# Kernel tuning notes

Measured on AMD Instinct MI355X. Metric: run time of the kernel, lower is better.

## Reference

```python
import jax, jax.numpy as jnp
import numpy as np

B, S, C, H, W = 8, 64, 3, 224, 224   # batch, n_segments, channels, height, width
E, P = 128, 16                        # embed_dim, patch size of feature extractor


def _conv(x, w, b, stride, padding):
    y = jax.lax.conv_general_dilated(
        x, w, (stride, stride), padding,
        dimension_numbers=('NCHW', 'OIHW', 'NCHW'))
    return y + b[None, :, None, None]


def setup_inputs() -> dict:
    key = jax.random.key(0)
    k1, k2, k3 = jax.random.split(key, 3)
    img = jax.random.normal(k1, (B, C, H, W), jnp.float32)
    # SpixelNet stand-in: 3x3 conv -> n_segments logit channels
    w_spixel = jax.random.normal(k2, (S, C, 3, 3), jnp.float32) * 0.1
    b_spixel = jnp.zeros((S,), jnp.float32)
    # feature extractor stand-in: 16x16/16 patch conv -> embed_dim, then GAP
    w_patch = jax.random.normal(k3, (E, C, P, P), jnp.float32) * 0.02
    b_patch = jnp.zeros((E,), jnp.float32)
    return dict(img=img, w_spixel=w_spixel, b_spixel=b_spixel,
                w_patch=w_patch, b_patch=b_patch)


def reference(img, w_spixel, b_spixel, w_patch, b_patch):
    # superpixel tokenizer -> segment logits, argmax -> hard labels
    logits = _conv(img, w_spixel, b_spixel, 1, 'SAME')          # [B,S,H,W]
    labels = jnp.argmax(logits, axis=1)                          # [B,H,W] int

    # replicate per-batch torch.unique (sorted unique labels, zero-padded)
    flat = labels.reshape(B, -1)
    present = jnp.zeros((B, S), bool).at[jnp.arange(B)[:, None], flat].set(True)
    vals = jnp.where(present, jnp.arange(S)[None, :], S)
    uniq = jnp.sort(vals, axis=1)                                # uniques first
    uniq = jnp.where(uniq < S, uniq, 0)                          # pad with 0 like torch.zeros

    # broadcast-compare mask build + masked extract (the memory-bound op)
    mask = (labels[:, None, :, :] == uniq[:, :, None, None]).astype(img.dtype)  # [B,S,H,W]
    seg = (img[:, None, :, :, :] * mask[:, :, None, :, :]).reshape(B * S, C, H, W)

    # feature extractor: patch conv + global average pool
    feat = _conv(seg, w_patch, b_patch, P, 'VALID')              # [B*S,E,H/P,W/P]
    feat = feat.mean(axis=(2, 3))                                # [B*S,E]
    return feat.reshape(B, S, E)
```

## Files before the change

### kernel.cpp

```cpp
#include <hip/hip_runtime.h>

#define BD 8
#define SD 64
#define CD 3
#define HD 224
#define WD 224
#define ED 128
#define PD 16
#define HWD (HD*WD)
#define KD (CD*PD*PD)
#define PRT 8
#define CHK (HWD/PRT)

__device__ float              g_part[BD * CD * PRT * SD * 256];
__device__ int                g_labels[BD * HWD];
__device__ unsigned long long g_ppres[BD * PRT];

__global__ __launch_bounds__(256) void k_labels(
    const float* __restrict__ img,
    const float* __restrict__ wsp,
    const float* __restrict__ bsp)
{
    const int p = blockIdx.x * 256 + threadIdx.x;
    const int b = blockIdx.y;
    const int h = p / WD;
    const int w = p - h * WD;

    const float* ib = img + (size_t)b * CD * HWD;
    float pix[27];
    #pragma unroll
    for (int c = 0; c < 3; ++c)
        #pragma unroll
        for (int dh = 0; dh < 3; ++dh)
            #pragma unroll
            for (int dw = 0; dw < 3; ++dw) {
                int hh = h + dh - 1, ww = w + dw - 1;
                bool ok = (hh >= 0) & (hh < HD) & (ww >= 0) & (ww < WD);
                pix[(c * 3 + dh) * 3 + dw] = ok ? ib[c * HWD + hh * WD + ww] : 0.f;
            }

    float best = -INFINITY;
    int bi = 0;
    for (int s = 0; s < SD; ++s) {
        const float* wr = wsp + s * 27;
        float acc = bsp[s];
        #pragma unroll
        for (int j = 0; j < 27; ++j) acc = fmaf(pix[j], wr[j], acc);
        if (acc > best) { best = acc; bi = s; }
    }
    g_labels[b * HWD + p] = bi;
}

__global__ __launch_bounds__(256) void k_hist(const float* __restrict__ img)
{
    const int part = blockIdx.x, c = blockIdx.y, b = blockIdx.z;
    const int tid = threadIdx.x;

    __shared__ float acc[SD * 256];
    __shared__ unsigned long long pm;
    #pragma unroll
    for (int k = 0; k < 16; ++k)
        ((float4*)acc)[k * 256 + tid] = make_float4(0.f, 0.f, 0.f, 0.f);
    if (tid == 0) pm = 0ull;
    __syncthreads();

    const int start = part * CHK;
    const int*   lb = g_labels + (size_t)b * HWD;
    const float* ic = img + ((size_t)b * CD + c) * HWD;

    unsigned long long m = 0ull;
    for (int p = start + tid; p < start + CHK; p += 256) {
        const int lab = lb[p];
        const int h = p / WD, w = p - h * WD;
        const int cell = ((h & 15) << 4) | (w & 15);
        atomicAdd(&acc[lab * 256 + cell], ic[p]);
        m |= 1ull << lab;
    }
    #pragma unroll
    for (int d = 1; d < 64; d <<= 1) m |= __shfl_xor(m, d, 64);
    if ((tid & 63) == 0) atomicOr(&pm, m);
    __syncthreads();

    float4* dst = (float4*)(g_part + (((size_t)(b * CD + c)) * PRT + part) * (SD * 256));
    #pragma unroll
    for (int k = 0; k < 16; ++k)
        dst[k * 256 + tid] = ((float4*)acc)[k * 256 + tid];
    if (c == 0 && tid == 0) g_ppres[b * PRT + part] = pm;
}

__global__ __launch_bounds__(256) void k_out(
    const float* __restrict__ wp,
    const float* __restrict__ bp,
    float* __restrict__ out)
{
    __shared__ float4 gs4[KD / 4];
    const int i = blockIdx.x;
    const int b = blockIdx.y;
    const int tid = threadIdx.x;
    const int lane = tid & 63;
    const int wv = tid >> 6;

    unsigned long long m = 0ull;
    #pragma unroll
    for (int p2 = 0; p2 < PRT; ++p2) m |= g_ppres[b * PRT + p2];

    int l = 0;
    if (i < __popcll(m)) {
        unsigned long long mm = m;
        for (int t = 0; t < i; ++t) mm &= mm - 1;
        l = __builtin_ctzll(mm);
    }

    if (tid < KD / 4) {
        const int c = tid >> 6, cell4 = tid & 63;
        const float4* src = (const float4*)g_part
            + ((size_t)(b * CD + c) * PRT) * 4096 + l * 64 + cell4;
        float4 s = src[0];
        #pragma unroll
        for (int p2 = 1; p2 < PRT; ++p2) {
            float4 v = src[(size_t)p2 * 4096];
            s.x += v.x; s.y += v.y; s.z += v.z; s.w += v.w;
        }
        gs4[tid] = s;
    }
    __syncthreads();

    const float4 g0 = gs4[lane], g1 = gs4[lane + 64], g2 = gs4[lane + 128];

    #pragma unroll 4
    for (int j = 0; j < 32; ++j) {
        const int e = wv * 32 + j;
        const float4* wr = (const float4*)(wp + (size_t)e * KD);
        float4 a0 = wr[lane], a1 = wr[lane + 64], a2 = wr[lane + 128];
        float acc = g0.x * a0.x;
        acc = fmaf(g0.y, a0.y, acc); acc = fmaf(g0.z, a0.z, acc); acc = fmaf(g0.w, a0.w, acc);
        acc = fmaf(g1.x, a1.x, acc); acc = fmaf(g1.y, a1.y, acc);
        acc = fmaf(g1.z, a1.z, acc); acc = fmaf(g1.w, a1.w, acc);
        acc = fmaf(g2.x, a2.x, acc); acc = fmaf(g2.y, a2.y, acc);
        acc = fmaf(g2.z, a2.z, acc); acc = fmaf(g2.w, a2.w, acc);
        #pragma unroll
        for (int off = 32; off; off >>= 1) acc += __shfl_xor(acc, off, 64);
        if (lane == 0)
            out[(size_t)(b * SD + i) * ED + e] = bp[e] + acc * (1.f / 196.f);
    }
}

extern "C" void kernel_launch(void* const* d_in, const int* in_sizes, int n_in,
                              void* d_out, int out_size, void* d_ws, size_t ws_size,
                              hipStream_t stream) {
    const float *img = nullptr, *wsp = nullptr, *bsp = nullptr, *wp = nullptr, *bp = nullptr;
    for (int i = 0; i < n_in; ++i) {
        switch (in_sizes[i]) {
            case BD * CD * HWD:      img = (const float*)d_in[i]; break;
            case SD * CD * 9:        wsp = (const float*)d_in[i]; break;
            case SD:                 bsp = (const float*)d_in[i]; break;
            case ED * CD * PD * PD:  wp  = (const float*)d_in[i]; break;
            case ED:                 bp  = (const float*)d_in[i]; break;
        }
    }
    float* out = (float*)d_out;

    dim3 g1(HWD / 256, BD, 1);
    k_labels<<<g1, 256, 0, stream>>>(img, wsp, bsp);

    dim3 g2(PRT, CD, BD);
    k_hist<<<g2, 256, 0, stream>>>(img);

    dim3 g3(SD, BD, 1);
    k_out<<<g3, 256, 0, stream>>>(wp, bp, out);
}
```

Baseline: 134.0 us.

## Pack label conv weights in LDS with dual FMA, prefetch hist loads, split output GEMV

The label kernel now stages the spixel weights and biases in shared memory, interleaved in pairs so two segments are evaluated per iteration with packed two-wide FMAs. This cuts scalar weight loads and arithmetic instructions in the argmax loop. The histogram loop software-prefetches the next label and pixel value to hide global load latency behind the LDS atomics. The output kernel splits the embedding dimension across two blocks in z, doubling the grid for more parallelism at the cost of each block redundantly re-reducing the partial histograms.

```diff
diff --git a/kernel.cpp b/kernel.cpp
--- a/kernel.cpp
+++ b/kernel.cpp
@@ -12,6 +12,8 @@
 #define PRT 8
 #define CHK (HWD/PRT)
 
+typedef float v2f __attribute__((ext_vector_type(2)));
+
 __device__ float              g_part[BD * CD * PRT * SD * 256];
 __device__ int                g_labels[BD * HWD];
 __device__ unsigned long long g_ppres[BD * PRT];
@@ -21,7 +23,17 @@
     const float* __restrict__ wsp,
     const float* __restrict__ bsp)
 {
-    const int p = blockIdx.x * 256 + threadIdx.x;
+    __shared__ __align__(16) float w_s[(SD / 2) * 56];
+    const int tid = threadIdx.x;
+    #pragma unroll
+    for (int t = tid; t < (SD / 2) * 56; t += 256) {
+        const int q = t / 56, r = t - q * 56;
+        const int j = r >> 1, s = 2 * q + (r & 1);
+        w_s[t] = (j < 27) ? wsp[s * 27 + j] : bsp[s];
+    }
+    __syncthreads();
+
+    const int p = blockIdx.x * 256 + tid;
     const int b = blockIdx.y;
     const int h = p / WD;
     const int w = p - h * WD;
@@ -39,14 +51,20 @@
                 pix[(c * 3 + dh) * 3 + dw] = ok ? ib[c * HWD + hh * WD + ww] : 0.f;
             }
 
+    v2f pd[27];
+    #pragma unroll
+    for (int j = 0; j < 27; ++j) { pd[j].x = pix[j]; pd[j].y = pix[j]; }
+
     float best = -INFINITY;
     int bi = 0;
-    for (int s = 0; s < SD; ++s) {
-        const float* wr = wsp + s * 27;
-        float acc = bsp[s];
+    for (int q = 0; q < SD / 2; ++q) {
+        const v2f* wrow = (const v2f*)w_s + q * 28;
+        v2f acc = wrow[27];
         #pragma unroll
-        for (int j = 0; j < 27; ++j) acc = fmaf(pix[j], wr[j], acc);
-        if (acc > best) { best = acc; bi = s; }
+        for (int j = 0; j < 27; ++j)
+            acc = __builtin_elementwise_fma(pd[j], wrow[j], acc);
+        if (acc.x > best) { best = acc.x; bi = 2 * q; }
+        if (acc.y > best) { best = acc.y; bi = 2 * q + 1; }
     }
     g_labels[b * HWD + p] = bi;
 }
@@ -65,16 +83,23 @@
     __syncthreads();
 
     const int start = part * CHK;
+    const int end   = start + CHK;
     const int*   lb = g_labels + (size_t)b * HWD;
     const float* ic = img + ((size_t)b * CD + c) * HWD;
 
     unsigned long long m = 0ull;
-    for (int p = start + tid; p < start + CHK; p += 256) {
-        const int lab = lb[p];
+    int p = start + tid;
+    int   lab = (p < end) ? lb[p] : 0;
+    float val = (p < end) ? ic[p] : 0.f;
+    while (p < end) {
+        const int pn = p + 256;
+        const int   labn = (pn < end) ? lb[pn] : 0;
+        const float valn = (pn < end) ? ic[pn] : 0.f;
         const int h = p / WD, w = p - h * WD;
         const int cell = ((h & 15) << 4) | (w & 15);
-        atomicAdd(&acc[lab * 256 + cell], ic[p]);
+        atomicAdd(&acc[lab * 256 + cell], val);
         m |= 1ull << lab;
+        p = pn; lab = labn; val = valn;
     }
     #pragma unroll
     for (int d = 1; d < 64; d <<= 1) m |= __shfl_xor(m, d, 64);
@@ -96,6 +121,7 @@
     __shared__ float4 gs4[KD / 4];
     const int i = blockIdx.x;
     const int b = blockIdx.y;
+    const int z = blockIdx.z;
     const int tid = threadIdx.x;
     const int lane = tid & 63;
     const int wv = tid >> 6;
@@ -128,8 +154,8 @@
     const float4 g0 = gs4[lane], g1 = gs4[lane + 64], g2 = gs4[lane + 128];
 
     #pragma unroll 4
-    for (int j = 0; j < 32; ++j) {
-        const int e = wv * 32 + j;
+    for (int j = 0; j < 16; ++j) {
+        const int e = z * 64 + wv * 16 + j;
         const float4* wr = (const float4*)(wp + (size_t)e * KD);
         float4 a0 = wr[lane], a1 = wr[lane + 64], a2 = wr[lane + 128];
         float acc = g0.x * a0.x;
@@ -166,6 +192,6 @@
     dim3 g2(PRT, CD, BD);
     k_hist<<<g2, 256, 0, stream>>>(img);
 
-    dim3 g3(SD, BD, 1);
+    dim3 g3(SD, BD, 2);
     k_out<<<g3, 256, 0, stream>>>(wp, bp, out);
 }
```

Measured after the change: 121.4 us. -9.4%, faster.
